# Performance work log

Measured on AMD Instinct MI355X. Metric: run time of the kernel, lower is better.

Reference implementation:

```python
import jax, jax.numpy as jnp
import numpy as np

B, S, D = 4, 2048, 1024
H = 2 * D          # hidden_dim = 2*n_embd
A = H // 16        # adapt_dim = 128
E = 8              # num_experts
K = 2              # top-k within group
GS = 4             # group_size
G = E // GS        # num_groups


def _ln(x, g, b, eps=1e-5):
    m = x.mean(-1, keepdims=True)
    v = x.var(-1, keepdims=True)
    return (x - m) / jnp.sqrt(v + eps) * g + b


def setup_inputs() -> dict:
    key = jax.random.key(0)
    ks = jax.random.split(key, 12)
    s = 1.0 / np.sqrt(D)       # shared MLP init scale
    sa = s * 0.01              # adapt layers init scale
    se = 0.01 / np.sqrt(A)     # expert adapter init scale
    f32 = jnp.float32
    return {
        "x": jax.random.normal(ks[0], (B, S, D), f32),
        "W_up": jax.random.normal(ks[1], (H, D), f32) * s,
        "W_gate": jax.random.normal(ks[2], (H, D), f32) * s,
        "W_down": jax.random.normal(ks[3], (D, H), f32) * s,
        "W_pre": jax.random.normal(ks[4], (A, D), f32) * sa,
        "W_post": jax.random.normal(ks[5], (A, H), f32) * sa,
        "g_an": jnp.ones((A,), f32),
        "b_an": jnp.zeros((A,), f32),
        "W_aproj": jax.random.normal(ks[6], (H, A), f32) * sa,
        "W_eadapt": jax.random.normal(ks[7], (E, A, A), f32) * se,
        "g_e": jnp.ones((E, A), f32),
        "b_e": jnp.zeros((E, A), f32),
        "W_eproj": jax.random.normal(ks[8], (H, A), f32) * se,
        "W_oproj": jax.random.normal(ks[9], (D, H), f32) * se,
        "W_rg": jax.random.normal(ks[10], (G, D), f32) * 0.001,
        "W_re": jax.random.normal(ks[11], (GS, D), f32) * 0.001,
    }


def reference(x, W_up, W_gate, W_down, W_pre, W_post, g_an, b_an, W_aproj,
              W_eadapt, g_e, b_e, W_eproj, W_oproj, W_rg, W_re):
    Bs, Ss, Ds = x.shape
    N = Bs * Ss
    xf = x.reshape(N, Ds)

    # ---- HierarchicalRouter ----
    gl = xf @ W_rg.T                                   # [N, G]
    gp = jax.nn.softmax(gl, axis=-1)
    gw = gp.max(axis=-1)                               # top-1 group weight
    gi = gp.argmax(axis=-1)                            # top-1 group index
    ll = xf @ W_re.T                                   # [N, GS]
    lp = jax.nn.softmax(ll, axis=-1)
    lw, li = jax.lax.top_k(lp, K)                      # [N, K]
    eidx = gi[:, None] * GS + li                       # global expert ids
    lw = lw / (lw.sum(-1, keepdims=True) + 1e-7)
    fw = gw[:, None] * lw                              # final weights [N, K]
    dispatch = jnp.zeros((N, E), x.dtype).at[jnp.arange(N)[:, None], eidx].set(fw)
    load = dispatch.sum(0)
    target = load.sum() / E
    load_balance_loss = jnp.mean((load - target) ** 2)
    z_loss = jnp.mean(gl ** 2) + jnp.mean(ll ** 2)
    router_loss = 0.001 * (load_balance_loss + z_loss)

    # ---- SharedExpertMLP ----
    up = x @ W_up.T                                    # [B, S, H]
    gate = x @ W_gate.T
    hidden = jax.nn.silu(gate) * up
    pre = x @ W_pre.T                                  # [B, S, A]
    a_in = _ln(pre, g_an, b_an)
    a_out = _ln(hidden @ W_post.T, g_an, b_an)
    aw = jax.nn.silu(jnp.clip(jnp.einsum('bsa,bta->bst', a_in, a_out), -5.0, 5.0))
    adapt = jnp.einsum('bst,bta->bsa', aw, a_in) @ W_aproj.T  # [B, S, H]
    hidden = hidden + 0.1 * adapt
    shared = hidden @ W_down.T                         # [B, S, D]

    # ---- ExpertGroup (vectorized gather/MLP/scatter) ----
    # sum_i w_i * (shared + 0.1*contrib_i) = shared*sum(w) + 0.1*sum_i w_i*contrib_i
    w = dispatch.reshape(Bs, Ss, E)                    # dispatch weights
    he = jnp.einsum('bsa,eca->ebsc', pre, W_eadapt)    # [E, B, S, A]
    he = _ln(he, g_e[:, None, None, :], b_e[:, None, None, :])
    wh = jnp.einsum('ebsa,bse->bsa', he, w)            # weighted combine at adapt_dim
    contrib = (wh @ W_eproj.T) @ W_oproj.T             # [B, S, D]
    out = shared * w.sum(-1, keepdims=True) + 0.1 * contrib
    return out, router_loss
```

## Files before the change

kernel.cpp:

```cpp
#include <hip/hip_runtime.h>
#include <hip/hip_bf16.h>

typedef unsigned short u16;
typedef short bf16x8 __attribute__((ext_vector_type(8)));
typedef float f32x4 __attribute__((ext_vector_type(4)));

#define N_TOK 8192
#define DIM   1024
#define HID   2048
#define ADIM  128
#define SEQ   2048
#define LDP   2304

__device__ __forceinline__ u16 f2bf_bits(float f){
  unsigned u = __float_as_uint(f);
  unsigned r = (u + 0x7fffu + ((u >> 16) & 1u)) >> 16;
  return (u16)r;
}
__device__ __forceinline__ float bf2f(u16 v){ return __uint_as_float((unsigned)v << 16); }
__device__ __forceinline__ float siluf(float x){ return x / (1.f + __expf(-x)); }

__device__ __forceinline__ void gload16(const void* g, void* l){
  __builtin_amdgcn_global_load_lds((const __attribute__((address_space(1))) void*)g,
                                   (__attribute__((address_space(3))) void*)l, 16, 0, 0);
}

#define SB0() __builtin_amdgcn_sched_barrier(0)

__global__ void __launch_bounds__(512, 2)
gemm_gu256(const u16* __restrict__ X, const u16* __restrict__ Wgu,
           const float* __restrict__ sumw, u16* __restrict__ hidP)
{
  extern __shared__ u16 lds[];
  const int tid = threadIdx.x, w = tid >> 6, lane = tid & 63;
  const int wm = w >> 2, wn = w & 3;
  const int xcd = blockIdx.x & 7, lloc = blockIdx.x >> 3;
  const int bm = (xcd >> 1) * 8 + (lloc & 7);
  const int bn = (xcd & 1) * 8 + (lloc >> 3);
  const long brow = (long)bm * 256, bcol = (long)bn * 256;
  const int frow = lane & 15;
  const int fks = ((lane >> 4) * 8) ^ (((lane >> 1) & 3) << 3);
  const int srow = lane >> 2;
  const int sslot = (((lane & 3) ^ ((lane >> 3) & 3)) * 8);

  f32x4 acc[8][4];
  #pragma unroll
  for (int m = 0; m < 8; m++)
    #pragma unroll
    for (int n = 0; n < 4; n++)
      #pragma unroll
      for (int i = 0; i < 4; i++) acc[m][n][i] = 0.f;

  auto stage = [&](const u16* __restrict__ gbase, long row0, int kt, int kh,
                   int p, int regoff) {
    #pragma unroll
    for (int i = 0; i < 2; i++) {
      const int r = (i * 8 + w) * 16 + srow;
      const u16* g = gbase + (row0 + r) * 1024 + kt * 64 + kh * 32 + sslot;
      u16* l = &lds[p * 32768 + regoff + kh * 8192 + (i * 8 + w) * 512];
      gload16(g, l);
    }
  };

#define AFRAG(mf, kss) (*(const bf16x8*)&lds[p*32768 + (kss)*8192 + (wm*128 + (mf)*16 + frow)*32 + fks])
#define BFRAG(nf, kss) (*(const bf16x8*)&lds[p*32768 + 16384 + (kss)*8192 + (wn*64 + (nf)*16 + frow)*32 + fks])

  stage(X, brow, 0, 0, 0, 0);
  stage(Wgu, bcol, 0, 0, 0, 16384);
  stage(X, brow, 0, 1, 0, 0);
  stage(Wgu, bcol, 0, 1, 0, 16384);
  asm volatile("s_waitcnt vmcnt(4)" ::: "memory");
  __builtin_amdgcn_s_barrier();

  for (int kt = 0; kt < 16; ++kt) {
    const int p = kt & 1, pn = p ^ 1;
    const int ktn = (kt < 15) ? kt + 1 : 15;
    bf16x8 b[4], a[4];

    a[0] = AFRAG(0, 0);
    b[0] = BFRAG(0, 0); b[1] = BFRAG(1, 0); b[2] = BFRAG(2, 0); b[3] = BFRAG(3, 0);
    SB0();
    a[1] = AFRAG(1, 0); SB0();
    a[2] = AFRAG(2, 0); SB0();
    a[3] = AFRAG(3, 0);
    stage(X, brow, ktn, 0, pn, 0);
    __builtin_amdgcn_s_barrier();
    asm volatile("s_waitcnt lgkmcnt(3)" ::: "memory"); SB0();
    __builtin_amdgcn_s_setprio(1);
    #pragma unroll
    for (int n = 0; n < 4; n++)
      acc[0][n] = __builtin_amdgcn_mfma_f32_16x16x32_bf16(a[0], b[n], acc[0][n], 0, 0, 0);
    asm volatile("s_waitcnt lgkmcnt(2)" ::: "memory"); SB0();
    #pragma unroll
    for (int n = 0; n < 4; n++)
      acc[1][n] = __builtin_amdgcn_mfma_f32_16x16x32_bf16(a[1], b[n], acc[1][n], 0, 0, 0);
    asm volatile("s_waitcnt lgkmcnt(1)" ::: "memory"); SB0();
    #pragma unroll
    for (int n = 0; n < 4; n++)
      acc[2][n] = __builtin_amdgcn_mfma_f32_16x16x32_bf16(a[2], b[n], acc[2][n], 0, 0, 0);
    asm volatile("s_waitcnt lgkmcnt(0)" ::: "memory"); SB0();
    #pragma unroll
    for (int n = 0; n < 4; n++)
      acc[3][n] = __builtin_amdgcn_mfma_f32_16x16x32_bf16(a[3], b[n], acc[3][n], 0, 0, 0);
    __builtin_amdgcn_s_setprio(0);
    __builtin_amdgcn_s_barrier();

    a[0] = AFRAG(4, 0); SB0();
    a[1] = AFRAG(5, 0); SB0();
    a[2] = AFRAG(6, 0); SB0();
    a[3] = AFRAG(7, 0);
    stage(Wgu, bcol, ktn, 0, pn, 16384);
    __builtin_amdgcn_s_barrier();
    asm volatile("s_waitcnt lgkmcnt(3)" ::: "memory"); SB0();
    __builtin_amdgcn_s_setprio(1);
    #pragma unroll
    for (int n = 0; n < 4; n++)
      acc[4][n] = __builtin_amdgcn_mfma_f32_16x16x32_bf16(a[0], b[n], acc[4][n], 0, 0, 0);
    asm volatile("s_waitcnt lgkmcnt(2)" ::: "memory"); SB0();
    #pragma unroll
    for (int n = 0; n < 4; n++)
      acc[5][n] = __builtin_amdgcn_mfma_f32_16x16x32_bf16(a[1], b[n], acc[5][n], 0, 0, 0);
    asm volatile("s_waitcnt lgkmcnt(1)" ::: "memory"); SB0();
    #pragma unroll
    for (int n = 0; n < 4; n++)
      acc[6][n] = __builtin_amdgcn_mfma_f32_16x16x32_bf16(a[2], b[n], acc[6][n], 0, 0, 0);
    asm volatile("s_waitcnt lgkmcnt(0)" ::: "memory"); SB0();
    #pragma unroll
    for (int n = 0; n < 4; n++)
      acc[7][n] = __builtin_amdgcn_mfma_f32_16x16x32_bf16(a[3], b[n], acc[7][n], 0, 0, 0);
    __builtin_amdgcn_s_setprio(0);
    asm volatile("s_waitcnt vmcnt(4)" ::: "memory");
    __builtin_amdgcn_s_barrier();

    a[0] = AFRAG(0, 1);
    b[0] = BFRAG(0, 1); b[1] = BFRAG(1, 1); b[2] = BFRAG(2, 1); b[3] = BFRAG(3, 1);
    SB0();
    a[1] = AFRAG(1, 1); SB0();
    a[2] = AFRAG(2, 1); SB0();
    a[3] = AFRAG(3, 1);
    stage(X, brow, ktn, 1, pn, 0);
    __builtin_amdgcn_s_barrier();
    asm volatile("s_waitcnt lgkmcnt(3)" ::: "memory"); SB0();
    __builtin_amdgcn_s_setprio(1);
    #pragma unroll
    for (int n = 0; n < 4; n++)
      acc[0][n] = __builtin_amdgcn_mfma_f32_16x16x32_bf16(a[0], b[n], acc[0][n], 0, 0, 0);
    asm volatile("s_waitcnt lgkmcnt(2)" ::: "memory"); SB0();
    #pragma unroll
    for (int n = 0; n < 4; n++)
      acc[1][n] = __builtin_amdgcn_mfma_f32_16x16x32_bf16(a[1], b[n], acc[1][n], 0, 0, 0);
    asm volatile("s_waitcnt lgkmcnt(1)" ::: "memory"); SB0();
    #pragma unroll
    for (int n = 0; n < 4; n++)
      acc[2][n] = __builtin_amdgcn_mfma_f32_16x16x32_bf16(a[2], b[n], acc[2][n], 0, 0, 0);
    asm volatile("s_waitcnt lgkmcnt(0)" ::: "memory"); SB0();
    #pragma unroll
    for (int n = 0; n < 4; n++)
      acc[3][n] = __builtin_amdgcn_mfma_f32_16x16x32_bf16(a[3], b[n], acc[3][n], 0, 0, 0);
    __builtin_amdgcn_s_setprio(0);
    __builtin_amdgcn_s_barrier();

    a[0] = AFRAG(4, 1); SB0();
    a[1] = AFRAG(5, 1); SB0();
    a[2] = AFRAG(6, 1); SB0();
    a[3] = AFRAG(7, 1);
    stage(Wgu, bcol, ktn, 1, pn, 16384);
    __builtin_amdgcn_s_barrier();
    asm volatile("s_waitcnt lgkmcnt(3)" ::: "memory"); SB0();
    __builtin_amdgcn_s_setprio(1);
    #pragma unroll
    for (int n = 0; n < 4; n++)
      acc[4][n] = __builtin_amdgcn_mfma_f32_16x16x32_bf16(a[0], b[n], acc[4][n], 0, 0, 0);
    asm volatile("s_waitcnt lgkmcnt(2)" ::: "memory"); SB0();
    #pragma unroll
    for (int n = 0; n < 4; n++)
      acc[5][n] = __builtin_amdgcn_mfma_f32_16x16x32_bf16(a[1], b[n], acc[5][n], 0, 0, 0);
    asm volatile("s_waitcnt lgkmcnt(1)" ::: "memory"); SB0();
    #pragma unroll
    for (int n = 0; n < 4; n++)
      acc[6][n] = __builtin_amdgcn_mfma_f32_16x16x32_bf16(a[2], b[n], acc[6][n], 0, 0, 0);
    asm volatile("s_waitcnt lgkmcnt(0)" ::: "memory"); SB0();
    #pragma unroll
    for (int n = 0; n < 4; n++)
      acc[7][n] = __builtin_amdgcn_mfma_f32_16x16x32_bf16(a[3], b[n], acc[7][n], 0, 0, 0);
    __builtin_amdgcn_s_setprio(0);
    asm volatile("s_waitcnt vmcnt(4)" ::: "memory");
    __builtin_amdgcn_s_barrier();
  }
#undef AFRAG
#undef BFRAG

  #pragma unroll
  for (int mf = 0; mf < 8; mf++)
    #pragma unroll
    for (int i = 0; i < 4; i++) {
      const long r = brow + wm * 128 + mf * 16 + (lane >> 4) * 4 + i;
      const float sw = sumw[r];
      #pragma unroll
      for (int q = 0; q < 2; q++) {
        const float g = acc[mf][2 * q][i], u = acc[mf][2 * q + 1][i];
        const int hcol = (bn * 8 + wn * 2 + q) * 16 + (lane & 15);
        hidP[r * LDP + hcol] = f2bf_bits(sw * (siluf(g) * u));
      }
    }
}

enum { EPI_BF16 = 0, EPI_SILU = 2 };

template<int EPI>
__global__ void __launch_bounds__(256, 2)
gemm_bt(const u16* __restrict__ Ag, const u16* __restrict__ Bg, int K, int lda, int ldb,
        long sAz, long sBz, long sOz, u16* __restrict__ bout, int ldo, int col0)
{
  __shared__ u16 lA[128 * 32];
  __shared__ u16 lB[128 * 32];
  const int tid = threadIdx.x, wave = tid >> 6, lane = tid & 63;
  const long brow = (long)blockIdx.y * 128, bcol = (long)blockIdx.x * 128;
  const u16* A = Ag + (long)blockIdx.z * sAz + brow * lda;
  const u16* B = Bg + (long)blockIdx.z * sBz + bcol * ldb;
  const int wr = (wave >> 1) * 64, wc = (wave & 1) * 64;

  f32x4 acc[4][4];
  #pragma unroll
  for (int m = 0; m < 4; m++)
    #pragma unroll
    for (int n = 0; n < 4; n++)
      #pragma unroll
      for (int i = 0; i < 4; i++) acc[m][n][i] = 0.f;

  const int sr = tid >> 2, sks = ((tid & 3) ^ ((tid >> 3) & 3)) * 8;
  const u16* gA = A + (long)sr * lda + sks;
  const u16* gB = B + (long)sr * ldb + sks;
  const long rA = (long)64 * lda, rB = (long)64 * ldb;
  u16* lA0 = &lA[wave * 512]; u16* lA1 = &lA[2048 + wave * 512];
  u16* lB0 = &lB[wave * 512]; u16* lB1 = &lB[2048 + wave * 512];
  const int frow = lane & 15;
  const int fks = ((lane >> 4) * 8) ^ (((lane >> 1) & 3) << 3);

  for (int kt = 0; kt < K; kt += 32) {
    gload16(gA, lA0); gload16(gA + rA, lA1);
    gload16(gB, lB0); gload16(gB + rB, lB1);
    gA += 32; gB += 32;
    asm volatile("s_waitcnt vmcnt(0)" ::: "memory");
    __syncthreads();
    bf16x8 af[4], bfv[4];
    #pragma unroll
    for (int m = 0; m < 4; m++) af[m] = *(const bf16x8*)&lA[(wr + m * 16 + frow) * 32 + fks];
    #pragma unroll
    for (int n = 0; n < 4; n++) bfv[n] = *(const bf16x8*)&lB[(wc + n * 16 + frow) * 32 + fks];
    #pragma unroll
    for (int m = 0; m < 4; m++)
      #pragma unroll
      for (int n = 0; n < 4; n++)
        acc[m][n] = __builtin_amdgcn_mfma_f32_16x16x32_bf16(af[m], bfv[n], acc[m][n], 0, 0, 0);
    __syncthreads();
  }

  const long r0 = brow + wr + ((lane >> 4) << 2);
  const long c0 = bcol + wc + (lane & 15);
  u16* O = bout + (long)blockIdx.z * sOz;
  #pragma unroll
  for (int m = 0; m < 4; m++) {
    #pragma unroll
    for (int i = 0; i < 4; i++) {
      long r = r0 + m * 16 + i;
      #pragma unroll
      for (int n = 0; n < 4; n++) {
        long c = c0 + n * 16;
        float v = acc[m][n][i];
        if constexpr (EPI == EPI_BF16) {
          O[r * ldo + col0 + c] = f2bf_bits(v);
        } else {
          v = fminf(5.f, fmaxf(-5.f, v));
          O[r * ldo + c] = f2bf_bits(siluf(v));
        }
      }
    }
  }
}

__global__ void __launch_bounds__(256, 2)
gemm_f32(const u16* __restrict__ Ag, const u16* __restrict__ Bg,
         float* __restrict__ out)
{
  __shared__ u16 lA[128 * 32];
  __shared__ u16 lB[128 * 32];
  const int tid = threadIdx.x, wave = tid >> 6, lane = tid & 63;
  const long brow = (long)blockIdx.y * 128, bcol = (long)blockIdx.x * 128;
  const int wr = (wave >> 1) * 64, wc = (wave & 1) * 64;

  f32x4 acc[4][4];
  #pragma unroll
  for (int m = 0; m < 4; m++)
    #pragma unroll
    for (int n = 0; n < 4; n++)
      #pragma unroll
      for (int i = 0; i < 4; i++) acc[m][n][i] = 0.f;

  const int sr = tid >> 2, sks = ((tid & 3) ^ ((tid >> 3) & 3)) * 8;
  const u16* gA = Ag + brow * LDP + (long)sr * LDP + sks;
  const u16* gB = Bg + bcol * LDP + (long)sr * LDP + sks;
  const long rA = (long)64 * LDP, rB = (long)64 * LDP;
  u16* lA0 = &lA[wave * 512]; u16* lA1 = &lA[2048 + wave * 512];
  u16* lB0 = &lB[wave * 512]; u16* lB1 = &lB[2048 + wave * 512];
  const int frow = lane & 15;
  const int fks = ((lane >> 4) * 8) ^ (((lane >> 1) & 3) << 3);

  for (int kt = 0; kt < LDP; kt += 32) {
    gload16(gA, lA0); gload16(gA + rA, lA1);
    gload16(gB, lB0); gload16(gB + rB, lB1);
    gA += 32; gB += 32;
    asm volatile("s_waitcnt vmcnt(0)" ::: "memory");
    __syncthreads();
    bf16x8 af[4], bfv[4];
    #pragma unroll
    for (int m = 0; m < 4; m++) af[m] = *(const bf16x8*)&lA[(wr + m * 16 + frow) * 32 + fks];
    #pragma unroll
    for (int n = 0; n < 4; n++) bfv[n] = *(const bf16x8*)&lB[(wc + n * 16 + frow) * 32 + fks];
    #pragma unroll
    for (int m = 0; m < 4; m++)
      #pragma unroll
      for (int n = 0; n < 4; n++)
        acc[m][n] = __builtin_amdgcn_mfma_f32_16x16x32_bf16(af[m], bfv[n], acc[m][n], 0, 0, 0);
    __syncthreads();
  }

  const long r0 = brow + wr + ((lane >> 4) << 2);
  const long c0 = bcol + wc + (lane & 15);
  #pragma unroll
  for (int m = 0; m < 4; m++)
    #pragma unroll
    for (int i = 0; i < 4; i++) {
      long r = r0 + m * 16 + i;
      #pragma unroll
      for (int n = 0; n < 4; n++)
        out[r * DIM + c0 + n * 16] = acc[m][n][i];
    }
}

__global__ void __launch_bounds__(256, 2)
gemm_split(const u16* __restrict__ Ag, const u16* __restrict__ Bg, int Ksub, int nsplit,
           int lda, int ldb, long sAz, long sBz, float* __restrict__ part)
{
  __shared__ u16 lA[128 * 32];
  __shared__ u16 lB[128 * 32];
  const int tid = threadIdx.x, wave = tid >> 6, lane = tid & 63;
  const int z = blockIdx.z, batch = z / nsplit, split = z % nsplit;
  const long brow = (long)blockIdx.y * 128;
  const int Mrows = gridDim.y * 128;
  const u16* A = Ag + (long)batch * sAz + brow * lda + (long)split * Ksub;
  const u16* B = Bg + (long)batch * sBz + (long)split * Ksub;
  const int wr = (wave >> 1) * 64, wc = (wave & 1) * 64;

  f32x4 acc[4][4];
  #pragma unroll
  for (int m = 0; m < 4; m++)
    #pragma unroll
    for (int n = 0; n < 4; n++)
      #pragma unroll
      for (int i = 0; i < 4; i++) acc[m][n][i] = 0.f;

  const int sr = tid >> 2, sks = ((tid & 3) ^ ((tid >> 3) & 3)) * 8;
  const u16* gA = A + (long)sr * lda + sks;
  const u16* gB = B + (long)sr * ldb + sks;
  const long rA = (long)64 * lda, rB = (long)64 * ldb;
  u16* lA0 = &lA[wave * 512]; u16* lA1 = &lA[2048 + wave * 512];
  u16* lB0 = &lB[wave * 512]; u16* lB1 = &lB[2048 + wave * 512];
  const int frow = lane & 15;
  const int fks = ((lane >> 4) * 8) ^ (((lane >> 1) & 3) << 3);

  for (int kt = 0; kt < Ksub; kt += 32) {
    gload16(gA, lA0); gload16(gA + rA, lA1);
    gload16(gB, lB0); gload16(gB + rB, lB1);
    gA += 32; gB += 32;
    asm volatile("s_waitcnt vmcnt(0)" ::: "memory");
    __syncthreads();
    bf16x8 af[4], bfv[4];
    #pragma unroll
    for (int m = 0; m < 4; m++) af[m] = *(const bf16x8*)&lA[(wr + m * 16 + frow) * 32 + fks];
    #pragma unroll
    for (int n = 0; n < 4; n++) bfv[n] = *(const bf16x8*)&lB[(wc + n * 16 + frow) * 32 + fks];
    #pragma unroll
    for (int m = 0; m < 4; m++)
      #pragma unroll
      for (int n = 0; n < 4; n++)
        acc[m][n] = __builtin_amdgcn_mfma_f32_16x16x32_bf16(af[m], bfv[n], acc[m][n], 0, 0, 0);
    __syncthreads();
  }

  float* po = part + (long)z * Mrows * 128;
  const long rr = brow + wr + ((lane >> 4) << 2);
  const int cc = wc + (lane & 15);
  #pragma unroll
  for (int m = 0; m < 4; m++)
    #pragma unroll
    for (int i = 0; i < 4; i++) {
      long r = rr + m * 16 + i;
      #pragma unroll
      for (int n = 0; n < 4; n++)
        po[r * 128 + cc + n * 16] = acc[m][n][i];
    }
}

__global__ void __launch_bounds__(256, 2)
gemm_split_q(const u16* __restrict__ A0, const u16* __restrict__ B0, int lda0,
             const u16* __restrict__ A1, const u16* __restrict__ B1, int lda1,
             float* __restrict__ part)
{
  __shared__ u16 lA[128 * 32];
  __shared__ u16 lB[128 * 32];
  const int tid = threadIdx.x, wave = tid >> 6, lane = tid & 63;
  const int z = blockIdx.z, sel = z >> 2, split = z & 3;
  const long brow = (long)blockIdx.y * 128;
  const int lda = sel ? lda1 : lda0;
  const u16* A = (sel ? A1 : A0) + brow * lda + (long)split * 512;
  const u16* B = (sel ? B1 : B0) + (long)split * 512;

  const int wr = (wave >> 1) * 64, wc = (wave & 1) * 64;
  f32x4 acc[4][4];
  #pragma unroll
  for (int m = 0; m < 4; m++)
    #pragma unroll
    for (int n = 0; n < 4; n++)
      #pragma unroll
      for (int i = 0; i < 4; i++) acc[m][n][i] = 0.f;

  const int sr = tid >> 2, sks = ((tid & 3) ^ ((tid >> 3) & 3)) * 8;
  const u16* gA = A + (long)sr * lda + sks;
  const u16* gB = B + (long)sr * HID + sks;
  const long rA = (long)64 * lda, rB = (long)64 * HID;
  u16* lA0 = &lA[wave * 512]; u16* lA1 = &lA[2048 + wave * 512];
  u16* lB0 = &lB[wave * 512]; u16* lB1 = &lB[2048 + wave * 512];
  const int frow = lane & 15;
  const int fks = ((lane >> 4) * 8) ^ (((lane >> 1) & 3) << 3);

  for (int kt = 0; kt < 512; kt += 32) {
    gload16(gA, lA0); gload16(gA + rA, lA1);
    gload16(gB, lB0); gload16(gB + rB, lB1);
    gA += 32; gB += 32;
    asm volatile("s_waitcnt vmcnt(0)" ::: "memory");
    __syncthreads();
    bf16x8 af[4], bfv[4];
    #pragma unroll
    for (int m = 0; m < 4; m++) af[m] = *(const bf16x8*)&lA[(wr + m * 16 + frow) * 32 + fks];
    #pragma unroll
    for (int n = 0; n < 4; n++) bfv[n] = *(const bf16x8*)&lB[(wc + n * 16 + frow) * 32 + fks];
    #pragma unroll
    for (int m = 0; m < 4; m++)
      #pragma unroll
      for (int n = 0; n < 4; n++)
        acc[m][n] = __builtin_amdgcn_mfma_f32_16x16x32_bf16(af[m], bfv[n], acc[m][n], 0, 0, 0);
    __syncthreads();
  }

  float* po = part + (long)z * 131072;
  const long rr = brow + wr + ((lane >> 4) << 2);
  const int cc = wc + (lane & 15);
  #pragma unroll
  for (int m = 0; m < 4; m++)
    #pragma unroll
    for (int i = 0; i < 4; i++) {
      long r = rr + m * 16 + i;
      #pragma unroll
      for (int n = 0; n < 4; n++)
        po[r * 128 + cc + n * 16] = acc[m][n][i];
    }
}

__global__ void __launch_bounds__(256)
prep_all(const float* __restrict__ x, const float* __restrict__ Wrg,
         const float* __restrict__ Wre, float* __restrict__ sumw,
         float* __restrict__ fwv, int* __restrict__ eidxv,
         float* __restrict__ stats, u16* __restrict__ xb,
         const float* __restrict__ Wg, const float* __restrict__ Wu,
         const float* __restrict__ Wd, const float* __restrict__ Wo,
         const float* __restrict__ Wpost, const float* __restrict__ Wpre,
         const float* __restrict__ Wead,
         u16* __restrict__ Wgu, u16* __restrict__ WdQ,
         u16* __restrict__ Wob, u16* __restrict__ Wpostb,
         u16* __restrict__ Wpreb, u16* __restrict__ Weadb,
         const float* __restrict__ Wa, const float* __restrict__ We,
         u16* __restrict__ Ta, u16* __restrict__ Te)
{
  __shared__ float lst[10];
  const int blk = blockIdx.x;
  if (blk < 512) {
    if (threadIdx.x < 10) lst[threadIdx.x] = 0.f;
    __syncthreads();
    const int wave = threadIdx.x >> 6, lane = threadIdx.x & 63;
    const float4* wg0 = (const float4*)Wrg;
    const float4* wg1 = (const float4*)(Wrg + 1024);
    const float4* we0 = (const float4*)Wre;
    const float4* we1 = (const float4*)(Wre + 1024);
    const float4* we2 = (const float4*)(Wre + 2048);
    const float4* we3 = (const float4*)(Wre + 3072);
    for (int t = 0; t < 4; t++) {
      const long n = (long)blk * 16 + wave * 4 + t;
      const float4* xr = (const float4*)(x + n * 1024);
      float d0 = 0, d1 = 0, t0 = 0, t1 = 0, t2 = 0, t3 = 0;
      #pragma unroll
      for (int j = 0; j < 4; j++) {
        int id = j * 64 + lane;
        float4 xv = xr[id];
        ushort4 xc;
        xc.x = f2bf_bits(xv.x); xc.y = f2bf_bits(xv.y);
        xc.z = f2bf_bits(xv.z); xc.w = f2bf_bits(xv.w);
        *(ushort4*)(xb + n * 1024 + id * 4) = xc;
        float4 a;
        a = wg0[id]; d0 += xv.x * a.x + xv.y * a.y + xv.z * a.z + xv.w * a.w;
        a = wg1[id]; d1 += xv.x * a.x + xv.y * a.y + xv.z * a.z + xv.w * a.w;
        a = we0[id]; t0 += xv.x * a.x + xv.y * a.y + xv.z * a.z + xv.w * a.w;
        a = we1[id]; t1 += xv.x * a.x + xv.y * a.y + xv.z * a.z + xv.w * a.w;
        a = we2[id]; t2 += xv.x * a.x + xv.y * a.y + xv.z * a.z + xv.w * a.w;
        a = we3[id]; t3 += xv.x * a.x + xv.y * a.y + xv.z * a.z + xv.w * a.w;
      }
      #pragma unroll
      for (int o = 32; o; o >>= 1) {
        d0 += __shfl_xor(d0, o); d1 += __shfl_xor(d1, o);
        t0 += __shfl_xor(t0, o); t1 += __shfl_xor(t1, o);
        t2 += __shfl_xor(t2, o); t3 += __shfl_xor(t3, o);
      }
      if (lane == 0) {
        float mg = fmaxf(d0, d1);
        float e0 = __expf(d0 - mg), e1 = __expf(d1 - mg);
        float invg = 1.f / (e0 + e1);
        float p0 = e0 * invg, p1 = e1 * invg;
        int gi = (d1 > d0) ? 1 : 0;
        float gw = fmaxf(p0, p1);
        float l[4] = {t0, t1, t2, t3};
        float ml = fmaxf(fmaxf(l[0], l[1]), fmaxf(l[2], l[3]));
        float p[4]; float su = 0;
        #pragma unroll
        for (int i = 0; i < 4; i++) { p[i] = __expf(l[i] - ml); su += p[i]; }
        float isu = 1.f / su;
        #pragma unroll
        for (int i = 0; i < 4; i++) p[i] *= isu;
        int i1 = 0;
        #pragma unroll
        for (int i = 1; i < 4; i++) if (p[i] > p[i1]) i1 = i;
        int i2 = (i1 == 0) ? 1 : 0;
        #pragma unroll
        for (int i = 0; i < 4; i++) if (i != i1 && p[i] > p[i2]) i2 = i;
        float s2 = p[i1] + p[i2];
        float invs = 1.f / (s2 + 1e-7f);
        float f1 = gw * p[i1] * invs, f2 = gw * p[i2] * invs;
        int ea = gi * 4 + i1, eb = gi * 4 + i2;
        sumw[n] = f1 + f2;
        fwv[2 * n] = f1; fwv[2 * n + 1] = f2;
        eidxv[2 * n] = ea; eidxv[2 * n + 1] = eb;
        atomicAdd(&lst[ea], f1);
        atomicAdd(&lst[eb], f2);
        atomicAdd(&lst[8], d0 * d0 + d1 * d1);
        atomicAdd(&lst[9], t0 * t0 + t1 * t1 + t2 * t2 + t3 * t3);
      }
    }
    __syncthreads();
    if (threadIdx.x < 10) atomicAdd(&stats[threadIdx.x], lst[threadIdx.x]);
  } else if (blk < 4864) {
    long i = ((long)(blk - 512) * 256 + threadIdx.x) * 8;
    const float* s; u16* d; long so, doff;
    if (i < 4194304) {
      long rp = i >> 10, c = i & 1023;
      long i32 = rp >> 5, wi = rp & 31;
      s = (wi < 16) ? Wg : Wu;
      so = (i32 * 16 + (wi & 15)) * 1024 + c;
      d = Wgu; doff = i;
    } else if (i < 6291456) {
      long j = i - 4194304;
      long r = j >> 11, c = j & 2047;
      s = Wd; so = j;
      d = WdQ; doff = r * LDP + c;
    } else if (i < 8388608) { s = Wo;    so = i - 6291456; d = Wob;    doff = so; }
    else if (i < 8650752)   { s = Wpost; so = i - 8388608; d = Wpostb; doff = so; }
    else if (i < 8781824)   { s = Wpre;  so = i - 8650752; d = Wpreb;  doff = so; }
    else                    { s = Wead;  so = i - 8781824; d = Weadb;  doff = so; }
    float4 v0 = *(const float4*)(s + so), v1 = *(const float4*)(s + so + 4);
    ushort4 p, q;
    p.x = f2bf_bits(v0.x); p.y = f2bf_bits(v0.y); p.z = f2bf_bits(v0.z); p.w = f2bf_bits(v0.w);
    q.x = f2bf_bits(v1.x); q.y = f2bf_bits(v1.y); q.z = f2bf_bits(v1.z); q.w = f2bf_bits(v1.w);
    *(ushort4*)(d + doff) = p;
    *(ushort4*)(d + doff + 4) = q;
  } else {
    int bid = blk - 4864;
    const float* src = (bid < 1024) ? Wa : We;
    u16* dst = (bid < 1024) ? Ta : Te;
    int idx = (bid & 1023) * 256 + threadIdx.x;
    int c = idx >> 11, r = idx & 2047;
    dst[idx] = f2bf_bits(src[(long)r * 128 + c]);
  }
}

__global__ void reduce_q(const float* __restrict__ part, u16* __restrict__ WdQ)
{
  int idx = blockIdx.x * 256 + threadIdx.x;
  int r = idx >> 8, c = idx & 255;
  const float* p = part + ((c < 128) ? 0 : 524288) + (long)r * 128 + (c & 127);
  float a = p[0] + p[131072] + p[262144] + p[393216];
  WdQ[(long)r * LDP + 2048 + c] = f2bf_bits(a);
}

__global__ void __launch_bounds__(256)
ln_rows_part(const float* __restrict__ part, int nsplit,
             const float* __restrict__ g, const float* __restrict__ b,
             const float* __restrict__ sumw,
             u16* __restrict__ out, u16* __restrict__ outT, u16* __restrict__ rawout)
{
  int wave = threadIdx.x >> 6, lane = threadIdx.x & 63;
  long n = (long)blockIdx.x * 4 + wave;
  long base = n * 128;
  float x0 = 0.f, x1 = 0.f;
  for (int s = 0; s < nsplit; s++) {
    x0 += part[(long)s * (N_TOK * ADIM) + base + lane];
    x1 += part[(long)s * (N_TOK * ADIM) + base + 64 + lane];
  }
  if (sumw) { float inv = 1.f / sumw[n]; x0 *= inv; x1 *= inv; }
  float s2 = x0 + x1, q = x0 * x0 + x1 * x1;
  #pragma unroll
  for (int o = 32; o; o >>= 1) { s2 += __shfl_xor(s2, o); q += __shfl_xor(q, o); }
  float m = s2 * (1.f / 128.f);
  float var = q * (1.f / 128.f) - m * m;
  float inv = rsqrtf(var + 1e-5f);
  float y0 = (x0 - m) * inv * g[lane] + b[lane];
  float y1 = (x1 - m) * inv * g[lane + 64] + b[lane + 64];
  out[base + lane] = f2bf_bits(y0);
  out[base + 64 + lane] = f2bf_bits(y1);
  if (outT) {
    long bb = n >> 11, ss = n & 2047;
    outT[(bb * 128 + lane) * 2048 + ss] = f2bf_bits(y0);
    outT[(bb * 128 + lane + 64) * 2048 + ss] = f2bf_bits(y1);
  }
  if (rawout) {
    rawout[base + lane] = f2bf_bits(x0);
    rawout[base + 64 + lane] = f2bf_bits(x1);
  }
}

__global__ void reduce_part_p1(const float* __restrict__ part,
                               const float* __restrict__ sumw, u16* __restrict__ hidP)
{
  int idx = blockIdx.x * 256 + threadIdx.x;
  int n = idx >> 5, c4 = (idx & 31) * 4;
  int batch = n >> 11, r = n & 2047;
  float4 a = {0.f, 0.f, 0.f, 0.f};
  #pragma unroll
  for (int s = 0; s < 4; s++) {
    float4 v = *(const float4*)(part + (((long)(batch * 4 + s) * 2048 + r) << 7) + c4);
    a.x += v.x; a.y += v.y; a.z += v.z; a.w += v.w;
  }
  float rs = 0.1f * sumw[n];
  ushort4 o;
  o.x = f2bf_bits(rs * a.x); o.y = f2bf_bits(rs * a.y);
  o.z = f2bf_bits(rs * a.z); o.w = f2bf_bits(rs * a.w);
  *(ushort4*)(hidP + (long)n * LDP + 2048 + c4) = o;
}

__global__ void init_stats(float* stats){ if (threadIdx.x < 16) stats[threadIdx.x] = 0.f; }

__global__ void finalize_loss(const float* __restrict__ stats, float* __restrict__ out)
{
  float tot = 0;
  #pragma unroll
  for (int e = 0; e < 8; e++) tot += stats[e];
  float target = tot * 0.125f;
  float lb = 0;
  #pragma unroll
  for (int e = 0; e < 8; e++) { float d = stats[e] - target; lb += d * d; }
  lb *= 0.125f;
  float z = stats[8] * (1.f / (8192.f * 2.f)) + stats[9] * (1.f / (8192.f * 4.f));
  out[0] = 0.001f * (lb + z);
}

__global__ void __launch_bounds__(256)
ln_combine(const u16* __restrict__ he, const int* __restrict__ eidxv,
           const float* __restrict__ fwv, const float* __restrict__ g_e,
           const float* __restrict__ b_e, u16* __restrict__ hidP)
{
  const int wave = threadIdx.x >> 6, lane = threadIdx.x & 63;
  const long n = (long)blockIdx.x * 4 + wave;
  float o0 = 0.f, o1 = 0.f;
  #pragma unroll
  for (int k = 0; k < 2; k++) {
    const int e = eidxv[2 * n + k];
    const float w = fwv[2 * n + k];
    const u16* row = he + ((long)e * N_TOK + n) * 128;
    float h0 = bf2f(row[lane]), h1 = bf2f(row[lane + 64]);
    float s = h0 + h1, q = h0 * h0 + h1 * h1;
    #pragma unroll
    for (int o = 32; o; o >>= 1) { s += __shfl_xor(s, o); q += __shfl_xor(q, o); }
    float m = s * (1.f / 128.f);
    float var = q * (1.f / 128.f) - m * m;
    float inv = rsqrtf(var + 1e-5f);
    o0 += w * ((h0 - m) * inv * g_e[e * 128 + lane] + b_e[e * 128 + lane]);
    o1 += w * ((h1 - m) * inv * g_e[e * 128 + lane + 64] + b_e[e * 128 + lane + 64]);
  }
  hidP[n * LDP + 2176 + lane] = f2bf_bits(0.1f * o0);
  hidP[n * LDP + 2176 + 64 + lane] = f2bf_bits(0.1f * o1);
}

extern "C" void kernel_launch(void* const* d_in, const int* in_sizes, int n_in,
                              void* d_out, int out_size, void* d_ws, size_t ws_size,
                              hipStream_t stream)
{
  (void)in_sizes; (void)n_in; (void)out_size; (void)ws_size;
  const float* x       = (const float*)d_in[0];
  const float* W_up    = (const float*)d_in[1];
  const float* W_gate  = (const float*)d_in[2];
  const float* W_down  = (const float*)d_in[3];
  const float* W_pre   = (const float*)d_in[4];
  const float* W_post  = (const float*)d_in[5];
  const float* g_an    = (const float*)d_in[6];
  const float* b_an    = (const float*)d_in[7];
  const float* W_aproj = (const float*)d_in[8];
  const float* W_ead   = (const float*)d_in[9];
  const float* g_e     = (const float*)d_in[10];
  const float* b_e     = (const float*)d_in[11];
  const float* W_eproj = (const float*)d_in[12];
  const float* W_oproj = (const float*)d_in[13];
  const float* W_rg    = (const float*)d_in[14];
  const float* W_re    = (const float*)d_in[15];
  float* out = (float*)d_out;

  char* base = (char*)d_ws; size_t off = 0;
  auto alloc = [&](size_t bytes) -> void* {
    void* p = base + off; off = (off + bytes + 255) & ~(size_t)255; return p;
  };
  u16*   xb     = (u16*)  alloc((size_t)N_TOK * DIM * 2);
  u16*   Wgu    = (u16*)  alloc((size_t)2 * HID * DIM * 2);
  u16*   WdQ    = (u16*)  alloc((size_t)DIM * LDP * 2);
  u16*   Wob    = (u16*)  alloc((size_t)DIM * HID * 2);
  u16*   Wpostb = (u16*)  alloc((size_t)ADIM * HID * 2);
  u16*   Wpreb  = (u16*)  alloc((size_t)ADIM * DIM * 2);
  u16*   WaTb   = (u16*)  alloc((size_t)ADIM * HID * 2);
  u16*   WeTb   = (u16*)  alloc((size_t)ADIM * HID * 2);
  u16*   Weadb  = (u16*)  alloc((size_t)8 * ADIM * ADIM * 2);
  u16*   hidP   = (u16*)  alloc((size_t)N_TOK * LDP * 2);
  u16*   heb    = (u16*)  alloc((size_t)8 * N_TOK * ADIM * 2);
  float* part   = (float*)heb;
  u16*   preb   = (u16*)  alloc((size_t)N_TOK * ADIM * 2);
  u16*   a_in   = (u16*)  alloc((size_t)N_TOK * ADIM * 2);
  u16*   a_inT  = (u16*)  alloc((size_t)N_TOK * ADIM * 2);
  u16*   a_out  = (u16*)  alloc((size_t)N_TOK * ADIM * 2);
  float* sumw   = (float*)alloc((size_t)N_TOK * 4);
  float* fwv    = (float*)alloc((size_t)N_TOK * 2 * 4);
  int*   eidxv  = (int*)  alloc((size_t)N_TOK * 2 * 4);
  float* stats  = (float*)alloc(64);
  u16* aw = (u16*)d_out;

  hipFuncSetAttribute((const void*)gemm_gu256,
                      hipFuncAttributeMaxDynamicSharedMemorySize, 131072);

  init_stats<<<1, 64, 0, stream>>>(stats);

  prep_all<<<6912, 256, 0, stream>>>(x, W_rg, W_re, sumw, fwv, eidxv, stats, xb,
                                     W_gate, W_up, W_down, W_oproj, W_post, W_pre,
                                     W_ead, Wgu, WdQ, Wob, Wpostb, Wpreb, Weadb,
                                     W_aproj, W_eproj, WaTb, WeTb);

  gemm_split_q<<<dim3(1, 8, 8), 256, 0, stream>>>(WdQ, WaTb, LDP, Wob, WeTb, HID, part);
  reduce_q<<<1024, 256, 0, stream>>>(part, WdQ);

  gemm_gu256<<<512, 512, 131072, stream>>>(xb, Wgu, sumw, hidP);

  gemm_split<<<dim3(1, 64, 4), 256, 0, stream>>>(xb, Wpreb, 256, 4, DIM, DIM, 0, 0, part);
  ln_rows_part<<<2048, 256, 0, stream>>>(part, 4, g_an, b_an, nullptr, a_in, a_inT, preb);

  gemm_bt<EPI_BF16><<<dim3(1, 64, 8), 256, 0, stream>>>(preb, Weadb, ADIM, ADIM, ADIM,
      0, (long)ADIM * ADIM, (long)N_TOK * ADIM, heb, ADIM, 0);
  ln_combine<<<2048, 256, 0, stream>>>(heb, eidxv, fwv, g_e, b_e, hidP);

  gemm_split<<<dim3(1, 64, 4), 256, 0, stream>>>(hidP, Wpostb, 512, 4, LDP, HID, 0, 0, part);
  ln_rows_part<<<2048, 256, 0, stream>>>(part, 4, g_an, b_an, sumw, a_out, nullptr, nullptr);

  gemm_bt<EPI_SILU><<<dim3(16, 16, 4), 256, 0, stream>>>(a_in, a_out, ADIM, ADIM, ADIM,
      (long)SEQ * ADIM, (long)SEQ * ADIM, (long)SEQ * SEQ, aw, SEQ, 0);

  gemm_split<<<dim3(1, 16, 16), 256, 0, stream>>>(aw, a_inT, 512, 4, SEQ, SEQ,
      (long)SEQ * SEQ, (long)ADIM * SEQ, part);
  reduce_part_p1<<<1024, 256, 0, stream>>>(part, sumw, hidP);

  gemm_f32<<<dim3(8, 64, 1), 256, 0, stream>>>(hidP, WdQ, out);

  finalize_loss<<<1, 1, 0, stream>>>(stats, out + (size_t)N_TOK * DIM);
}
```

Baseline: 269.9 us.

## Switch gate/up GEMM to 32x32x16 MFMA with 32-row interleaved weight layout

```diff
diff --git a/kernel.cpp b/kernel.cpp
--- a/kernel.cpp
+++ b/kernel.cpp
@@ -4,6 +4,7 @@
 typedef unsigned short u16;
 typedef short bf16x8 __attribute__((ext_vector_type(8)));
 typedef float f32x4 __attribute__((ext_vector_type(4)));
+typedef float f32x16 __attribute__((ext_vector_type(16)));
 
 #define N_TOK 8192
 #define DIM   1024
@@ -38,18 +39,19 @@
   const int bm = (xcd >> 1) * 8 + (lloc & 7);
   const int bn = (xcd & 1) * 8 + (lloc >> 3);
   const long brow = (long)bm * 256, bcol = (long)bn * 256;
-  const int frow = lane & 15;
-  const int fks = ((lane >> 4) * 8) ^ (((lane >> 1) & 3) << 3);
+  const int r32 = lane & 31;
+  const int khalf = lane >> 5;
+  const int fkey = (lane >> 1) & 3;
   const int srow = lane >> 2;
   const int sslot = (((lane & 3) ^ ((lane >> 3) & 3)) * 8);
 
-  f32x4 acc[8][4];
-  #pragma unroll
-  for (int m = 0; m < 8; m++)
-    #pragma unroll
-    for (int n = 0; n < 4; n++)
-      #pragma unroll
-      for (int i = 0; i < 4; i++) acc[m][n][i] = 0.f;
+  f32x16 acc[4][2];
+  #pragma unroll
+  for (int m = 0; m < 4; m++)
+    #pragma unroll
+    for (int n = 0; n < 2; n++)
+      #pragma unroll
+      for (int i = 0; i < 16; i++) acc[m][n][i] = 0.f;
 
   auto stage = [&](const u16* __restrict__ gbase, long row0, int kt, int kh,
                    int p, int regoff) {
@@ -62,8 +64,9 @@
     }
   };
 
-#define AFRAG(mf, kss) (*(const bf16x8*)&lds[p*32768 + (kss)*8192 + (wm*128 + (mf)*16 + frow)*32 + fks])
-#define BFRAG(nf, kss) (*(const bf16x8*)&lds[p*32768 + 16384 + (kss)*8192 + (wn*64 + (nf)*16 + frow)*32 + fks])
+#define AFRAG(mf, kh, ks) (*(const bf16x8*)&lds[p*32768 + (kh)*8192 + (wm*128 + (mf)*32 + r32)*32 + ((((ks)*2 + khalf) ^ fkey)*8)])
+#define BFRAG(nf, kh, ks) (*(const bf16x8*)&lds[p*32768 + 16384 + (kh)*8192 + (wn*64 + (nf)*32 + r32)*32 + ((((ks)*2 + khalf) ^ fkey)*8)])
+#define MFMA32(a_, b_, c_) __builtin_amdgcn_mfma_f32_32x32x16_bf16(a_, b_, c_, 0, 0, 0)
 
   stage(X, brow, 0, 0, 0, 0);
   stage(Wgu, bcol, 0, 0, 0, 16384);
@@ -75,134 +78,119 @@
   for (int kt = 0; kt < 16; ++kt) {
     const int p = kt & 1, pn = p ^ 1;
     const int ktn = (kt < 15) ? kt + 1 : 15;
-    bf16x8 b[4], a[4];
-
-    a[0] = AFRAG(0, 0);
-    b[0] = BFRAG(0, 0); b[1] = BFRAG(1, 0); b[2] = BFRAG(2, 0); b[3] = BFRAG(3, 0);
+    bf16x8 a0, a1, a2, a3, b[2][2];
+
+    a0 = AFRAG(0, 0, 0);
+    b[0][0] = BFRAG(0, 0, 0); b[1][0] = BFRAG(1, 0, 0);
+    b[0][1] = BFRAG(0, 0, 1); b[1][1] = BFRAG(1, 0, 1);
     SB0();
-    a[1] = AFRAG(1, 0); SB0();
-    a[2] = AFRAG(2, 0); SB0();
-    a[3] = AFRAG(3, 0);
+    a1 = AFRAG(0, 0, 1); SB0();
+    a2 = AFRAG(1, 0, 0); SB0();
+    a3 = AFRAG(1, 0, 1);
     stage(X, brow, ktn, 0, pn, 0);
     __builtin_amdgcn_s_barrier();
     asm volatile("s_waitcnt lgkmcnt(3)" ::: "memory"); SB0();
     __builtin_amdgcn_s_setprio(1);
-    #pragma unroll
-    for (int n = 0; n < 4; n++)
-      acc[0][n] = __builtin_amdgcn_mfma_f32_16x16x32_bf16(a[0], b[n], acc[0][n], 0, 0, 0);
+    acc[0][0] = MFMA32(a0, b[0][0], acc[0][0]);
+    acc[0][1] = MFMA32(a0, b[1][0], acc[0][1]);
     asm volatile("s_waitcnt lgkmcnt(2)" ::: "memory"); SB0();
-    #pragma unroll
-    for (int n = 0; n < 4; n++)
-      acc[1][n] = __builtin_amdgcn_mfma_f32_16x16x32_bf16(a[1], b[n], acc[1][n], 0, 0, 0);
+    acc[0][0] = MFMA32(a1, b[0][1], acc[0][0]);
+    acc[0][1] = MFMA32(a1, b[1][1], acc[0][1]);
     asm volatile("s_waitcnt lgkmcnt(1)" ::: "memory"); SB0();
-    #pragma unroll
-    for (int n = 0; n < 4; n++)
-      acc[2][n] = __builtin_amdgcn_mfma_f32_16x16x32_bf16(a[2], b[n], acc[2][n], 0, 0, 0);
+    acc[1][0] = MFMA32(a2, b[0][0], acc[1][0]);
+    acc[1][1] = MFMA32(a2, b[1][0], acc[1][1]);
     asm volatile("s_waitcnt lgkmcnt(0)" ::: "memory"); SB0();
-    #pragma unroll
-    for (int n = 0; n < 4; n++)
-      acc[3][n] = __builtin_amdgcn_mfma_f32_16x16x32_bf16(a[3], b[n], acc[3][n], 0, 0, 0);
+    acc[1][0] = MFMA32(a3, b[0][1], acc[1][0]);
+    acc[1][1] = MFMA32(a3, b[1][1], acc[1][1]);
     __builtin_amdgcn_s_setprio(0);
     __builtin_amdgcn_s_barrier();
 
-    a[0] = AFRAG(4, 0); SB0();
-    a[1] = AFRAG(5, 0); SB0();
-    a[2] = AFRAG(6, 0); SB0();
-    a[3] = AFRAG(7, 0);
+    a0 = AFRAG(2, 0, 0); SB0();
+    a1 = AFRAG(2, 0, 1); SB0();
+    a2 = AFRAG(3, 0, 0); SB0();
+    a3 = AFRAG(3, 0, 1);
     stage(Wgu, bcol, ktn, 0, pn, 16384);
     __builtin_amdgcn_s_barrier();
     asm volatile("s_waitcnt lgkmcnt(3)" ::: "memory"); SB0();
     __builtin_amdgcn_s_setprio(1);
-    #pragma unroll
-    for (int n = 0; n < 4; n++)
-      acc[4][n] = __builtin_amdgcn_mfma_f32_16x16x32_bf16(a[0], b[n], acc[4][n], 0, 0, 0);
+    acc[2][0] = MFMA32(a0, b[0][0], acc[2][0]);
+    acc[2][1] = MFMA32(a0, b[1][0], acc[2][1]);
     asm volatile("s_waitcnt lgkmcnt(2)" ::: "memory"); SB0();
-    #pragma unroll
-    for (int n = 0; n < 4; n++)
-      acc[5][n] = __builtin_amdgcn_mfma_f32_16x16x32_bf16(a[1], b[n], acc[5][n], 0, 0, 0);
+    acc[2][0] = MFMA32(a1, b[0][1], acc[2][0]);
+    acc[2][1] = MFMA32(a1, b[1][1], acc[2][1]);
     asm volatile("s_waitcnt lgkmcnt(1)" ::: "memory"); SB0();
-    #pragma unroll
-    for (int n = 0; n < 4; n++)
-      acc[6][n] = __builtin_amdgcn_mfma_f32_16x16x32_bf16(a[2], b[n], acc[6][n], 0, 0, 0);
+    acc[3][0] = MFMA32(a2, b[0][0], acc[3][0]);
+    acc[3][1] = MFMA32(a2, b[1][0], acc[3][1]);
     asm volatile("s_waitcnt lgkmcnt(0)" ::: "memory"); SB0();
-    #pragma unroll
-    for (int n = 0; n < 4; n++)
-      acc[7][n] = __builtin_amdgcn_mfma_f32_16x16x32_bf16(a[3], b[n], acc[7][n], 0, 0, 0);
+    acc[3][0] = MFMA32(a3, b[0][1], acc[3][0]);
+    acc[3][1] = MFMA32(a3, b[1][1], acc[3][1]);
     __builtin_amdgcn_s_setprio(0);
     asm volatile("s_waitcnt vmcnt(4)" ::: "memory");
     __builtin_amdgcn_s_barrier();
 
-    a[0] = AFRAG(0, 1);
-    b[0] = BFRAG(0, 1); b[1] = BFRAG(1, 1); b[2] = BFRAG(2, 1); b[3] = BFRAG(3, 1);
+    a0 = AFRAG(0, 1, 0);
+    b[0][0] = BFRAG(0, 1, 0); b[1][0] = BFRAG(1, 1, 0);
+    b[0][1] = BFRAG(0, 1, 1); b[1][1] = BFRAG(1, 1, 1);
     SB0();
-    a[1] = AFRAG(1, 1); SB0();
-    a[2] = AFRAG(2, 1); SB0();
-    a[3] = AFRAG(3, 1);
+    a1 = AFRAG(0, 1, 1); SB0();
+    a2 = AFRAG(1, 1, 0); SB0();
+    a3 = AFRAG(1, 1, 1);
     stage(X, brow, ktn, 1, pn, 0);
     __builtin_amdgcn_s_barrier();
     asm volatile("s_waitcnt lgkmcnt(3)" ::: "memory"); SB0();
     __builtin_amdgcn_s_setprio(1);
-    #pragma unroll
-    for (int n = 0; n < 4; n++)
-      acc[0][n] = __builtin_amdgcn_mfma_f32_16x16x32_bf16(a[0], b[n], acc[0][n], 0, 0, 0);
+    acc[0][0] = MFMA32(a0, b[0][0], acc[0][0]);
+    acc[0][1] = MFMA32(a0, b[1][0], acc[0][1]);
     asm volatile("s_waitcnt lgkmcnt(2)" ::: "memory"); SB0();
-    #pragma unroll
-    for (int n = 0; n < 4; n++)
-      acc[1][n] = __builtin_amdgcn_mfma_f32_16x16x32_bf16(a[1], b[n], acc[1][n], 0, 0, 0);
+    acc[0][0] = MFMA32(a1, b[0][1], acc[0][0]);
+    acc[0][1] = MFMA32(a1, b[1][1], acc[0][1]);
     asm volatile("s_waitcnt lgkmcnt(1)" ::: "memory"); SB0();
-    #pragma unroll
-    for (int n = 0; n < 4; n++)
-      acc[2][n] = __builtin_amdgcn_mfma_f32_16x16x32_bf16(a[2], b[n], acc[2][n], 0, 0, 0);
+    acc[1][0] = MFMA32(a2, b[0][0], acc[1][0]);
+    acc[1][1] = MFMA32(a2, b[1][0], acc[1][1]);
     asm volatile("s_waitcnt lgkmcnt(0)" ::: "memory"); SB0();
-    #pragma unroll
-    for (int n = 0; n < 4; n++)
-      acc[3][n] = __builtin_amdgcn_mfma_f32_16x16x32_bf16(a[3], b[n], acc[3][n], 0, 0, 0);
+    acc[1][0] = MFMA32(a3, b[0][1], acc[1][0]);
+    acc[1][1] = MFMA32(a3, b[1][1], acc[1][1]);
     __builtin_amdgcn_s_setprio(0);
     __builtin_amdgcn_s_barrier();
 
-    a[0] = AFRAG(4, 1); SB0();
-    a[1] = AFRAG(5, 1); SB0();
-    a[2] = AFRAG(6, 1); SB0();
-    a[3] = AFRAG(7, 1);
+    a0 = AFRAG(2, 1, 0); SB0();
+    a1 = AFRAG(2, 1, 1); SB0();
+    a2 = AFRAG(3, 1, 0); SB0();
+    a3 = AFRAG(3, 1, 1);
     stage(Wgu, bcol, ktn, 1, pn, 16384);
     __builtin_amdgcn_s_barrier();
     asm volatile("s_waitcnt lgkmcnt(3)" ::: "memory"); SB0();
     __builtin_amdgcn_s_setprio(1);
-    #pragma unroll
-    for (int n = 0; n < 4; n++)
-      acc[4][n] = __builtin_amdgcn_mfma_f32_16x16x32_bf16(a[0], b[n], acc[4][n], 0, 0, 0);
+    acc[2][0] = MFMA32(a0, b[0][0], acc[2][0]);
+    acc[2][1] = MFMA32(a0, b[1][0], acc[2][1]);
     asm volatile("s_waitcnt lgkmcnt(2)" ::: "memory"); SB0();
-    #pragma unroll
-    for (int n = 0; n < 4; n++)
-      acc[5][n] = __builtin_amdgcn_mfma_f32_16x16x32_bf16(a[1], b[n], acc[5][n], 0, 0, 0);
+    acc[2][0] = MFMA32(a1, b[0][1], acc[2][0]);
+    acc[2][1] = MFMA32(a1, b[1][1], acc[2][1]);
     asm volatile("s_waitcnt lgkmcnt(1)" ::: "memory"); SB0();
-    #pragma unroll
-    for (int n = 0; n < 4; n++)
-      acc[6][n] = __builtin_amdgcn_mfma_f32_16x16x32_bf16(a[2], b[n], acc[6][n], 0, 0, 0);
+    acc[3][0] = MFMA32(a2, b[0][0], acc[3][0]);
+    acc[3][1] = MFMA32(a2, b[1][0], acc[3][1]);
     asm volatile("s_waitcnt lgkmcnt(0)" ::: "memory"); SB0();
-    #pragma unroll
-    for (int n = 0; n < 4; n++)
-      acc[7][n] = __builtin_amdgcn_mfma_f32_16x16x32_bf16(a[3], b[n], acc[7][n], 0, 0, 0);
+    acc[3][0] = MFMA32(a3, b[0][1], acc[3][0]);
+    acc[3][1] = MFMA32(a3, b[1][1], acc[3][1]);
     __builtin_amdgcn_s_setprio(0);
     asm volatile("s_waitcnt vmcnt(4)" ::: "memory");
     __builtin_amdgcn_s_barrier();
   }
 #undef AFRAG
 #undef BFRAG
-
-  #pragma unroll
-  for (int mf = 0; mf < 8; mf++)
-    #pragma unroll
-    for (int i = 0; i < 4; i++) {
-      const long r = brow + wm * 128 + mf * 16 + (lane >> 4) * 4 + i;
+#undef MFMA32
+
+  #pragma unroll
+  for (int mf = 0; mf < 4; mf++) {
+    #pragma unroll
+    for (int reg = 0; reg < 16; reg++) {
+      const long r = brow + wm * 128 + mf * 32 + (reg & 3) + 8 * (reg >> 2) + 4 * khalf;
       const float sw = sumw[r];
-      #pragma unroll
-      for (int q = 0; q < 2; q++) {
-        const float g = acc[mf][2 * q][i], u = acc[mf][2 * q + 1][i];
-        const int hcol = (bn * 8 + wn * 2 + q) * 16 + (lane & 15);
-        hidP[r * LDP + hcol] = f2bf_bits(sw * (siluf(g) * u));
-      }
+      const float g = acc[mf][0][reg], u = acc[mf][1][reg];
+      const int hcol = bn * 128 + wn * 32 + r32;
+      hidP[r * LDP + hcol] = f2bf_bits(sw * (siluf(g) * u));
     }
+  }
 }
 
 enum { EPI_BF16 = 0, EPI_SILU = 2 };
@@ -561,9 +549,9 @@
     const float* s; u16* d; long so, doff;
     if (i < 4194304) {
       long rp = i >> 10, c = i & 1023;
-      long i32 = rp >> 5, wi = rp & 31;
-      s = (wi < 16) ? Wg : Wu;
-      so = (i32 * 16 + (wi & 15)) * 1024 + c;
+      long i64 = rp >> 6, wi = rp & 63;
+      s = (wi < 32) ? Wg : Wu;
+      so = (i64 * 32 + (wi & 31)) * 1024 + c;
       d = Wgu; doff = i;
     } else if (i < 6291456) {
       long j = i - 4194304;
@@ -653,8 +641,6 @@
   o.z = f2bf_bits(rs * a.z); o.w = f2bf_bits(rs * a.w);
   *(ushort4*)(hidP + (long)n * LDP + 2048 + c4) = o;
 }
-
-__global__ void init_stats(float* stats){ if (threadIdx.x < 16) stats[threadIdx.x] = 0.f; }
 
 __global__ void finalize_loss(const float* __restrict__ stats, float* __restrict__ out)
 {
@@ -749,7 +735,7 @@
   hipFuncSetAttribute((const void*)gemm_gu256,
                       hipFuncAttributeMaxDynamicSharedMemorySize, 131072);
 
-  init_stats<<<1, 64, 0, stream>>>(stats);
+  hipMemsetAsync(stats, 0, 64, stream);
 
   prep_all<<<6912, 256, 0, stream>>>(x, W_rg, W_re, sumw, fwv, eidxv, stats, xb,
                                      W_gate, W_up, W_down, W_oproj, W_post, W_pre,
```

Measured after the change: 277.1 us. 1.03x slower.
